# Performance work log

Measured on AMD Instinct MI355X. Metric: run time of the kernel, lower is better.

Reference implementation:

```python
import jax, jax.numpy as jnp
import numpy as np

CLIP = 7.0          # cfg.swiglu_clip
AUX_COEF = 0.02     # cfg.router_aux_loss_coef
TOP_K = 4           # cfg.experts_per_token


def setup_inputs() -> dict:
    key = jax.random.key(0)
    ks = jax.random.split(key, 4)
    H, E, FF = 1024, 16, 1024
    B, T = 2, 1024
    std = 0.02
    return {
        "x": jax.random.normal(ks[0], (B, T, H), jnp.float32),
        "W_in": jax.random.normal(ks[1], (E, H, 2 * FF), jnp.float32) * std,
        "b_in": jnp.zeros((E, 2 * FF), jnp.float32),
        "W_out": jax.random.normal(ks[2], (E, FF, H), jnp.float32) * std,
        "b_out": jnp.zeros((E, H), jnp.float32),
        "router_w": jax.random.normal(ks[3], (E, H), jnp.float32) * std,
        "router_b": jnp.zeros((E,), jnp.float32),
    }


def reference(x, W_in, b_in, W_out, b_out, router_w, router_b):
    B, T, H = x.shape
    E = W_in.shape[0]
    S = B * T
    x_flat = x.reshape(S, H)

    # --- router + top-k gating ---
    logits = x_flat @ router_w.T + router_b                         # [S, E]
    topk_w, topk_i = jax.lax.top_k(logits, TOP_K)                   # [S, K]
    topk_w = jax.nn.softmax(topk_w.astype(jnp.float32), axis=-1).astype(x.dtype)

    # --- aux load-balance loss (faithful to source, incl. argmax-over-indices) ---
    probs = jax.nn.softmax(logits.astype(jnp.float32), axis=-1)     # [S, E]
    importance = probs.mean(axis=0)                                 # [E]
    load = jax.nn.one_hot(jnp.argmax(topk_i, axis=-1), E, dtype=jnp.float32).mean(axis=0)
    aux_loss = AUX_COEF * E * jnp.sum(importance * load)

    # scatter top-k weights to dense [S, E] combine weights
    final_w = jnp.zeros((S, E), x.dtype).at[jnp.arange(S)[:, None], topk_i].add(topk_w)

    # --- dense per-expert SwiGLU FFN (every expert for every token) ---
    h = jnp.einsum('sh,ehd->sed', x_flat, W_in) + b_in              # [S, E, 2*FF]
    up, gate = jnp.split(h, 2, axis=-1)                             # chunk(2, -1)
    up = jnp.clip(up, -CLIP, CLIP)
    gate = jnp.clip(gate, -CLIP, CLIP)
    act = jax.nn.silu(gate) * up                                    # [S, E, FF]
    eo = jnp.einsum('sef,efh->seh', act, W_out) + b_out             # [S, E, H]

    out = jnp.einsum('seh,se->sh', eo, final_w).reshape(B, T, H)
    return out, aux_loss
```

## Files before the change

### kernel.cpp

```cpp
#include <hip/hip_runtime.h>
#include <math.h>

#define S_TOK 2048
#define H_DIM 1024
#define E_NUM 16
#define FF_DIM 1024
#define TOPK 4
#define CLIPV 7.0f
#define AUXC 0.02f
#define BK 32
#define NT (H_DIM / BK)

typedef short bf16x8 __attribute__((ext_vector_type(8)));
typedef float f32x4 __attribute__((ext_vector_type(4)));

__device__ __forceinline__ unsigned short f2bf(float f) {
  unsigned int u = __float_as_uint(f);
  u += 0x7fffu + ((u >> 16) & 1u);
  return (unsigned short)(u >> 16);
}

__device__ __forceinline__ void gload16(const void* g, void* l) {
  __builtin_amdgcn_global_load_lds((const __attribute__((address_space(1))) void*)g,
                                   (__attribute__((address_space(3))) void*)l, 16, 0, 0);
}

__device__ __forceinline__ int imin(int a, int b) { return a < b ? a : b; }

__global__ void logits_kernel(const float* __restrict__ x, const float* __restrict__ rw,
                              const float* __restrict__ rb, float* __restrict__ logits,
                              unsigned short* __restrict__ xb) {
  int tok = blockIdx.x * 4 + (threadIdx.x >> 6);
  int lane = threadIdx.x & 63;
  const float4* xr = (const float4*)(x + (size_t)tok * H_DIM);
  ushort4* xbw = (ushort4*)(xb + (size_t)tok * H_DIM);
  float p[E_NUM];
#pragma unroll
  for (int e = 0; e < E_NUM; ++e) p[e] = 0.f;
#pragma unroll
  for (int it = 0; it < 4; ++it) {
    float4 xv = xr[it * 64 + lane];
    ushort4 o;
    o.x = f2bf(xv.x); o.y = f2bf(xv.y); o.z = f2bf(xv.z); o.w = f2bf(xv.w);
    xbw[it * 64 + lane] = o;
#pragma unroll
    for (int e = 0; e < E_NUM; ++e) {
      float4 wv = ((const float4*)(rw + (size_t)e * H_DIM))[it * 64 + lane];
      p[e] += xv.x * wv.x + xv.y * wv.y + xv.z * wv.z + xv.w * wv.w;
    }
  }
#pragma unroll
  for (int e = 0; e < E_NUM; ++e) {
#pragma unroll
    for (int off = 32; off > 0; off >>= 1) p[e] += __shfl_xor(p[e], off);
  }
  if (lane == 0) {
    float4* lp = (float4*)&logits[tok * E_NUM];
#pragma unroll
    for (int q = 0; q < 4; ++q)
      lp[q] = make_float4(p[q * 4 + 0] + rb[q * 4 + 0], p[q * 4 + 1] + rb[q * 4 + 1],
                          p[q * 4 + 2] + rb[q * 4 + 2], p[q * 4 + 3] + rb[q * 4 + 3]);
  }
}

__global__ __launch_bounds__(256) void topk_kernel(const float* __restrict__ logits,
                                                   int* __restrict__ topk_i, float* __restrict__ topk_w,
                                                   int* __restrict__ counts, float* __restrict__ imp,
                                                   int* __restrict__ pos_cnt) {
  __shared__ float s_imp[E_NUM];
  __shared__ int s_cnt[E_NUM];
  __shared__ int s_pos[TOPK];
  int tid = threadIdx.x;
  if (tid < E_NUM) { s_imp[tid] = 0.f; s_cnt[tid] = 0; }
  if (tid < TOPK) s_pos[tid] = 0;
  __syncthreads();

  int t = blockIdx.x * 256 + tid;
  float lg[E_NUM];
  {
    const float4* lp = (const float4*)&logits[t * E_NUM];
#pragma unroll
    for (int q = 0; q < 4; ++q) {
      float4 v = lp[q];
      lg[q * 4 + 0] = v.x; lg[q * 4 + 1] = v.y; lg[q * 4 + 2] = v.z; lg[q * 4 + 3] = v.w;
    }
  }
  int idx[TOPK]; float val[TOPK];
  float tmp[E_NUM];
#pragma unroll
  for (int e = 0; e < E_NUM; ++e) tmp[e] = lg[e];
#pragma unroll
  for (int k = 0; k < TOPK; ++k) {
    float best = -INFINITY; int bi = 0;
#pragma unroll
    for (int e = 0; e < E_NUM; ++e) if (tmp[e] > best) { best = tmp[e]; bi = e; }
    val[k] = best; idx[k] = bi; tmp[bi] = -INFINITY;
  }
  float ssum = 0.f, wv[TOPK];
#pragma unroll
  for (int k = 0; k < TOPK; ++k) { wv[k] = expf(val[k] - val[0]); ssum += wv[k]; }
#pragma unroll
  for (int k = 0; k < TOPK; ++k) wv[k] /= ssum;
#pragma unroll
  for (int k = 0; k < TOPK; ++k) {
    topk_i[t * TOPK + k] = idx[k];
    topk_w[t * TOPK + k] = wv[k];
  }
  float se = 0.f, pr[E_NUM];
#pragma unroll
  for (int e = 0; e < E_NUM; ++e) { pr[e] = expf(lg[e] - val[0]); se += pr[e]; }
  float inv = 1.f / se;
  int mi = idx[0], pos = 0;
#pragma unroll
  for (int k = 1; k < TOPK; ++k) if (idx[k] > mi) { mi = idx[k]; pos = k; }

  int lane = tid & 63;
#pragma unroll
  for (int e = 0; e < E_NUM; ++e) {
    float v = pr[e] * inv;
    int c = (idx[0] == e) + (idx[1] == e) + (idx[2] == e) + (idx[3] == e);
#pragma unroll
    for (int off = 32; off > 0; off >>= 1) {
      v += __shfl_xor(v, off);
      c += __shfl_xor(c, off);
    }
    if (lane == 0) {
      atomicAdd(&s_imp[e], v);
      atomicAdd(&s_cnt[e], c);
    }
  }
#pragma unroll
  for (int k = 0; k < TOPK; ++k) {
    int pc = (pos == k) ? 1 : 0;
#pragma unroll
    for (int off = 32; off > 0; off >>= 1) pc += __shfl_xor(pc, off);
    if (lane == 0) atomicAdd(&s_pos[k], pc);
  }
  __syncthreads();
  if (tid < E_NUM) {
    atomicAdd(&imp[tid], s_imp[tid]);
    atomicAdd(&counts[tid], s_cnt[tid]);
  }
  if (tid < TOPK) atomicAdd(&pos_cnt[tid], s_pos[tid]);
}

__global__ __launch_bounds__(256) void assign_kernel(
    const int* __restrict__ topk_i, const int* __restrict__ counts, int* __restrict__ cursor,
    int* __restrict__ tok_list, int* __restrict__ slot_of, int* __restrict__ offsets) {
  __shared__ int s_cnt[E_NUM];
  __shared__ int s_base[E_NUM];
  __shared__ int s_off[E_NUM + 1];
  int tid = threadIdx.x;
  if (tid == 0) {
    int o = 0;
    for (int e2 = 0; e2 < E_NUM; ++e2) { s_off[e2] = o; o += counts[e2]; }
    s_off[E_NUM] = o;
    if (blockIdx.x == 0) {
      for (int e2 = 0; e2 <= E_NUM; ++e2) offsets[e2] = s_off[e2];
    }
  }
  if (tid < E_NUM) s_cnt[tid] = 0;
  __syncthreads();
  int t = blockIdx.x * 256 + tid;
  int e[TOPK], lslot[TOPK];
#pragma unroll
  for (int k = 0; k < TOPK; ++k) {
    e[k] = topk_i[t * TOPK + k];
    lslot[k] = atomicAdd(&s_cnt[e[k]], 1);
  }
  __syncthreads();
  if (tid < E_NUM) s_base[tid] = atomicAdd(&cursor[tid], s_cnt[tid]);
  __syncthreads();
#pragma unroll
  for (int k = 0; k < TOPK; ++k) {
    int slot = s_off[e[k]] + s_base[e[k]] + lslot[k];
    tok_list[slot] = t;
    slot_of[t * TOPK + k] = slot;
  }
}

__global__ __launch_bounds__(256, 4) void transpose_fused_kernel(
    const float* __restrict__ W_in, unsigned short* __restrict__ winT,
    const float* __restrict__ W_out, unsigned short* __restrict__ woutT) {
  __shared__ unsigned int tile2[128][66];
  const int bid = blockIdx.x;
  const float* in;
  unsigned short* out;
  int C, r0, c0;
  if (bid < 2048) {
    int e = bid >> 7, rem = bid & 127;
    in  = W_in + (size_t)e * H_DIM * 2 * FF_DIM;
    out = winT + (size_t)e * H_DIM * 2 * FF_DIM;
    C = 2 * FF_DIM;
    r0 = (rem & 7) * 128;
    c0 = (rem >> 3) * 128;
  } else {
    int b = bid - 2048;
    int e = b >> 6, rem = b & 63;
    in  = W_out + (size_t)e * FF_DIM * H_DIM;
    out = woutT + (size_t)e * FF_DIM * H_DIM;
    C = H_DIM;
    r0 = (rem & 7) * 128;
    c0 = (rem >> 3) * 128;
  }
  const int t = threadIdx.x;
  const int tx = t & 31;
  const int ty = t >> 5;
#pragma unroll
  for (int j = 0; j < 8; ++j) {
    int rp = ty + j * 8;
    int r = rp * 2;
    float4 v0 = *(const float4*)&in[(size_t)(r0 + r) * C + c0 + tx * 4];
    float4 v1 = *(const float4*)&in[(size_t)(r0 + r + 1) * C + c0 + tx * 4];
    tile2[tx * 4 + 0][rp] = (unsigned)f2bf(v0.x) | ((unsigned)f2bf(v1.x) << 16);
    tile2[tx * 4 + 1][rp] = (unsigned)f2bf(v0.y) | ((unsigned)f2bf(v1.y) << 16);
    tile2[tx * 4 + 2][rp] = (unsigned)f2bf(v0.z) | ((unsigned)f2bf(v1.z) << 16);
    tile2[tx * 4 + 3][rp] = (unsigned)f2bf(v0.w) | ((unsigned)f2bf(v1.w) << 16);
  }
  __syncthreads();
  const int ux = t & 15;
  const int uy = t >> 4;
#pragma unroll
  for (int j = 0; j < 8; ++j) {
    int c = uy + j * 16;
    uint2 d0 = *(const uint2*)&tile2[c][ux * 4];
    uint2 d1 = *(const uint2*)&tile2[c][ux * 4 + 2];
    uint4 q = make_uint4(d0.x, d0.y, d1.x, d1.y);
    *(uint4*)&out[(size_t)(c0 + c) * 1024 + r0 + ux * 8] = q;
  }
}

__global__ __launch_bounds__(256, 6) void gemm1_kernel(
    const unsigned short* __restrict__ xb, const unsigned short* __restrict__ winT,
    const float* __restrict__ b_in, const int* __restrict__ offsets,
    const int* __restrict__ tok_list, unsigned short* __restrict__ act) {
  __shared__ unsigned short ldsA[2][128 * BK];
  __shared__ unsigned short ldsB[2][64 * BK];
  const int lin = blockIdx.x;
  const int nid = (lin & 7) * 1024 + (lin >> 3);
  const int e  = nid >> 9;
  const int nt = (nid >> 4) & 31;
  const int mt = nid & 15;
  const int base = offsets[e];
  const int cnt = offsets[e + 1] - base;
  if (mt * 128 >= cnt) return;
  const int n0f = nt * 32;
  const int tid = threadIdx.x, w = tid >> 6, lane = tid & 63;

  const int csrc = (lane & 3) ^ ((lane >> 3) & 3);
  const int arow = w * 16 + (lane >> 2);
  const int t0 = tok_list[base + imin(mt * 128 + arow, cnt - 1)];
  const int t1 = tok_list[base + imin(mt * 128 + arow + 64, cnt - 1)];
  const unsigned short* gA0 = xb + (size_t)t0 * H_DIM + csrc * 8;
  const unsigned short* gA1 = xb + (size_t)t1 * H_DIM + csrc * 8;
  const int rB = arow;
  const int fB = n0f + ((rB >> 5) << 4) + (rB & 15);
  const int wrow = ((rB >> 4) & 1) ? (FF_DIM + fB) : fB;
  const unsigned short* we = winT + (size_t)e * 2 * FF_DIM * H_DIM;
  const unsigned short* gB0 = we + (size_t)wrow * H_DIM + csrc * 8;

  f32x4 acc[4][2];
#pragma unroll
  for (int m = 0; m < 4; ++m)
#pragma unroll
    for (int n = 0; n < 2; ++n) acc[m][n] = (f32x4){0.f, 0.f, 0.f, 0.f};

#define STAGE1(buf, k0)                                        \
  do {                                                         \
    gload16(gA0 + (k0), &ldsA[buf][(w * 16) * BK]);            \
    gload16(gA1 + (k0), &ldsA[buf][(w * 16 + 64) * BK]);       \
    gload16(gB0 + (k0), &ldsB[buf][(w * 16) * BK]);            \
  } while (0)

  STAGE1(0, 0);
  __syncthreads();
  int buf = 0;
  const int kos = (((lane >> 4) ^ ((lane >> 1) & 3)) * 8);
  const int wm = (w >> 1) * 64, wn = (w & 1) * 32;
  for (int kt = 0; kt < NT; ++kt) {
    if (kt + 1 < NT) STAGE1(buf ^ 1, (kt + 1) * BK);
    bf16x8 a[4], b[2];
#pragma unroll
    for (int mf = 0; mf < 4; ++mf)
      a[mf] = *(const bf16x8*)&ldsA[buf][(wm + mf * 16 + (lane & 15)) * BK + kos];
#pragma unroll
    for (int nf = 0; nf < 2; ++nf)
      b[nf] = *(const bf16x8*)&ldsB[buf][(wn + nf * 16 + (lane & 15)) * BK + kos];
#pragma unroll
    for (int mf = 0; mf < 4; ++mf)
#pragma unroll
      for (int nf = 0; nf < 2; ++nf)
        acc[mf][nf] = __builtin_amdgcn_mfma_f32_16x16x32_bf16(a[mf], b[nf], acc[mf][nf], 0, 0, 0);
    __syncthreads();
    buf ^= 1;
  }

  const float* bin = b_in + (size_t)e * 2 * FF_DIM;
  const int f = n0f + (w & 1) * 16 + (lane & 15);
  const float bu = bin[f], bg = bin[FF_DIM + f];
#pragma unroll
  for (int mf = 0; mf < 4; ++mf) {
    int rbase = wm + mf * 16 + (lane >> 4) * 4;
#pragma unroll
    for (int i = 0; i < 4; ++i) {
      int mrow = mt * 128 + rbase + i;
      if (mrow < cnt) {
        float up = acc[mf][0][i] + bu;
        float gt = acc[mf][1][i] + bg;
        up = fminf(fmaxf(up, -CLIPV), CLIPV);
        gt = fminf(fmaxf(gt, -CLIPV), CLIPV);
        float av = (gt / (1.f + expf(-gt))) * up;
        act[(size_t)(base + mrow) * FF_DIM + f] = f2bf(av);
      }
    }
  }
}

__global__ __launch_bounds__(256, 4) void gemm2_kernel(
    const unsigned short* __restrict__ act, const unsigned short* __restrict__ woutT,
    const float* __restrict__ b_out, const int* __restrict__ offsets,
    float* __restrict__ eo) {
  __shared__ unsigned short ldsA[2][128 * BK];
  __shared__ unsigned short ldsB[2][128 * BK];
  const int lin = blockIdx.x;
  const int nid = (lin & 7) * 256 + (lin >> 3);
  const int e = nid >> 7;
  const int nt = (nid >> 4) & 7;
  const int mt = nid & 15;
  const int base = offsets[e];
  const int cnt = offsets[e + 1] - base;
  if (mt * 128 >= cnt) return;
  const int n0 = nt * 128;
  const int tid = threadIdx.x, w = tid >> 6, lane = tid & 63;

  const int csrc = (lane & 3) ^ ((lane >> 3) & 3);
  const int srow0 = w * 32 + (lane >> 2);
  const int srow1 = srow0 + 16;
  const int m0_ = imin(mt * 128 + srow0, cnt - 1);
  const int m1_ = imin(mt * 128 + srow1, cnt - 1);
  const unsigned short* gA0 = act + (size_t)(base + m0_) * FF_DIM + csrc * 8;
  const unsigned short* gA1 = act + (size_t)(base + m1_) * FF_DIM + csrc * 8;
  const unsigned short* we = woutT + (size_t)e * H_DIM * FF_DIM;
  const unsigned short* gB0 = we + (size_t)(n0 + srow0) * FF_DIM + csrc * 8;
  const unsigned short* gB1 = we + (size_t)(n0 + srow1) * FF_DIM + csrc * 8;

  f32x4 acc[4][4];
#pragma unroll
  for (int m = 0; m < 4; ++m)
#pragma unroll
    for (int n = 0; n < 4; ++n) acc[m][n] = (f32x4){0.f, 0.f, 0.f, 0.f};

#define STAGE2(buf, k0)                                        \
  do {                                                         \
    gload16(gA0 + (k0), &ldsA[buf][(w * 32 + 0) * BK]);        \
    gload16(gA1 + (k0), &ldsA[buf][(w * 32 + 16) * BK]);       \
    gload16(gB0 + (k0), &ldsB[buf][(w * 32 + 0) * BK]);        \
    gload16(gB1 + (k0), &ldsB[buf][(w * 32 + 16) * BK]);       \
  } while (0)

  STAGE2(0, 0);
  __syncthreads();
  int buf = 0;
  const int kos = (((lane >> 4) ^ ((lane >> 1) & 3)) * 8);
  const int wm = (w >> 1) * 64, wn = (w & 1) * 64;
  for (int kt = 0; kt < FF_DIM / BK; ++kt) {
    if (kt + 1 < FF_DIM / BK) STAGE2(buf ^ 1, (kt + 1) * BK);
    bf16x8 a[4], b[4];
#pragma unroll
    for (int mf = 0; mf < 4; ++mf)
      a[mf] = *(const bf16x8*)&ldsA[buf][(wm + mf * 16 + (lane & 15)) * BK + kos];
#pragma unroll
    for (int nf = 0; nf < 4; ++nf)
      b[nf] = *(const bf16x8*)&ldsB[buf][(wn + nf * 16 + (lane & 15)) * BK + kos];
#pragma unroll
    for (int mf = 0; mf < 4; ++mf)
#pragma unroll
      for (int nf = 0; nf < 4; ++nf)
        acc[mf][nf] = __builtin_amdgcn_mfma_f32_16x16x32_bf16(a[mf], b[nf], acc[mf][nf], 0, 0, 0);
    __syncthreads();
    buf ^= 1;
  }

  const float* bo = b_out + (size_t)e * H_DIM;
#pragma unroll
  for (int mf = 0; mf < 4; ++mf) {
#pragma unroll
    for (int i = 0; i < 4; ++i) {
      int mrow = mt * 128 + wm + mf * 16 + (lane >> 4) * 4 + i;
      if (mrow < cnt) {
        float* row = eo + (size_t)(base + mrow) * H_DIM;
#pragma unroll
        for (int nf = 0; nf < 4; ++nf) {
          int h = n0 + wn + nf * 16 + (lane & 15);
          row[h] = acc[mf][nf][i] + bo[h];
        }
      }
    }
  }
}

__global__ __launch_bounds__(256) void combine_kernel(
    const float* __restrict__ eo, const float* __restrict__ topk_w,
    const int* __restrict__ slot_of, float* __restrict__ out,
    const float* __restrict__ imp, const int* __restrict__ pos_cnt) {
  int t = blockIdx.x;
  int tid = threadIdx.x;
  float4 r = make_float4(0.f, 0.f, 0.f, 0.f);
#pragma unroll
  for (int k = 0; k < TOPK; ++k) {
    int s = slot_of[t * TOPK + k];
    float wv = topk_w[t * TOPK + k];
    float4 v = ((const float4*)(eo + (size_t)s * H_DIM))[tid];
    r.x = fmaf(wv, v.x, r.x);
    r.y = fmaf(wv, v.y, r.y);
    r.z = fmaf(wv, v.z, r.z);
    r.w = fmaf(wv, v.w, r.w);
  }
  ((float4*)(out + (size_t)t * H_DIM))[tid] = r;
  if (t == 0 && tid == 0) {
    float s = 0.f;
    for (int p = 0; p < TOPK; ++p)
      s += (imp[p] / (float)S_TOK) * ((float)pos_cnt[p] / (float)S_TOK);
    out[(size_t)S_TOK * H_DIM] = AUXC * (float)E_NUM * s;
  }
}

extern "C" void kernel_launch(void* const* d_in, const int* in_sizes, int n_in,
                              void* d_out, int out_size, void* d_ws, size_t ws_size,
                              hipStream_t stream) {
  const float* x     = (const float*)d_in[0];
  const float* W_in  = (const float*)d_in[1];
  const float* b_in  = (const float*)d_in[2];
  const float* W_out = (const float*)d_in[3];
  const float* b_out = (const float*)d_in[4];
  const float* rw    = (const float*)d_in[5];
  const float* rb    = (const float*)d_in[6];
  float* out = (float*)d_out;

  char* ws = (char*)d_ws;
  size_t off = 0;
  auto alloc = [&](size_t bytes) {
    void* p = ws + off;
    off = (off + bytes + 255) & ~(size_t)255;
    return p;
  };
  unsigned short* xb    = (unsigned short*)alloc((size_t)S_TOK * H_DIM * 2);
  unsigned short* winT  = (unsigned short*)alloc((size_t)E_NUM * 2 * FF_DIM * H_DIM * 2);
  unsigned short* woutT = (unsigned short*)alloc((size_t)E_NUM * H_DIM * FF_DIM * 2);
  unsigned short* act   = (unsigned short*)alloc((size_t)S_TOK * TOPK * FF_DIM * 2);
  float* eo      = (float*)alloc((size_t)S_TOK * TOPK * H_DIM * 4);
  float* logits  = (float*)alloc((size_t)S_TOK * E_NUM * 4);
  int*   topk_i  = (int*)alloc(S_TOK * TOPK * 4);
  float* topk_w  = (float*)alloc(S_TOK * TOPK * 4);
  int*   tok_list= (int*)alloc(S_TOK * TOPK * 4);
  int*   slot_of = (int*)alloc(S_TOK * TOPK * 4);
  int* ctrl = (int*)alloc(64 * 4);
  int* counts = ctrl;
  int* cursor = ctrl + 16;
  int* pos_cnt = ctrl + 32;
  float* imp = (float*)(ctrl + 48);
  int* offsets = (int*)alloc(32 * 4);

  hipMemsetAsync(ctrl, 0, 64 * 4, stream);

  transpose_fused_kernel<<<3072, 256, 0, stream>>>(W_in, winT, W_out, woutT);
  logits_kernel<<<S_TOK / 4, 256, 0, stream>>>(x, rw, rb, logits, xb);
  topk_kernel<<<S_TOK / 256, 256, 0, stream>>>(logits, topk_i, topk_w, counts, imp, pos_cnt);
  assign_kernel<<<S_TOK / 256, 256, 0, stream>>>(topk_i, counts, cursor, tok_list, slot_of, offsets);
  gemm1_kernel<<<8192, 256, 0, stream>>>(xb, winT, b_in, offsets, tok_list, act);
  gemm2_kernel<<<2048, 256, 0, stream>>>(act, woutT, b_out, offsets, eo);
  combine_kernel<<<S_TOK, 256, 0, stream>>>(eo, topk_w, slot_of, out, imp, pos_cnt);
}
```

Measured before the change: 200.5 us.

## Fuse W_in fp32-to-bf16 conversion into gemm1 and drop its transpose pass

gemm1 now loads the fp32 W_in tiles straight into LDS and converts them to bf16 while building the MFMA B fragments. This removes the separate transpose/convert pass over W_in and the round trip through the winT buffer. The W_out transpose becomes its own kernel launched after gemm1. In exchange, gemm1 reads fp32 weights, twice the bytes, and each active M-tile of an expert rereads them. It also does strided scalar LDS reads plus per-element conversion in the inner loop, and its occupancy hint drops from 6 to 4.

```diff
diff --git a/kernel.cpp b/kernel.cpp
--- a/kernel.cpp
+++ b/kernel.cpp
@@ -179,30 +179,16 @@
   }
 }
 
-__global__ __launch_bounds__(256, 4) void transpose_fused_kernel(
-    const float* __restrict__ W_in, unsigned short* __restrict__ winT,
+__global__ __launch_bounds__(256, 4) void transpose_wout_kernel(
     const float* __restrict__ W_out, unsigned short* __restrict__ woutT) {
   __shared__ unsigned int tile2[128][66];
-  const int bid = blockIdx.x;
-  const float* in;
-  unsigned short* out;
-  int C, r0, c0;
-  if (bid < 2048) {
-    int e = bid >> 7, rem = bid & 127;
-    in  = W_in + (size_t)e * H_DIM * 2 * FF_DIM;
-    out = winT + (size_t)e * H_DIM * 2 * FF_DIM;
-    C = 2 * FF_DIM;
-    r0 = (rem & 7) * 128;
-    c0 = (rem >> 3) * 128;
-  } else {
-    int b = bid - 2048;
-    int e = b >> 6, rem = b & 63;
-    in  = W_out + (size_t)e * FF_DIM * H_DIM;
-    out = woutT + (size_t)e * FF_DIM * H_DIM;
-    C = H_DIM;
-    r0 = (rem & 7) * 128;
-    c0 = (rem >> 3) * 128;
-  }
+  const int b = blockIdx.x;
+  const int e = b >> 6, rem = b & 63;
+  const float* in = W_out + (size_t)e * FF_DIM * H_DIM;
+  unsigned short* out = woutT + (size_t)e * FF_DIM * H_DIM;
+  const int C = H_DIM;
+  const int r0 = (rem & 7) * 128;
+  const int c0 = (rem >> 3) * 128;
   const int t = threadIdx.x;
   const int tx = t & 31;
   const int ty = t >> 5;
@@ -230,12 +216,12 @@
   }
 }
 
-__global__ __launch_bounds__(256, 6) void gemm1_kernel(
-    const unsigned short* __restrict__ xb, const unsigned short* __restrict__ winT,
+__global__ __launch_bounds__(256, 4) void gemm1_kernel(
+    const unsigned short* __restrict__ xb, const float* __restrict__ W_in,
     const float* __restrict__ b_in, const int* __restrict__ offsets,
     const int* __restrict__ tok_list, unsigned short* __restrict__ act) {
   __shared__ unsigned short ldsA[2][128 * BK];
-  __shared__ unsigned short ldsB[2][64 * BK];
+  __shared__ float ldsBf[2][32 * 64];
   const int lin = blockIdx.x;
   const int nid = (lin & 7) * 1024 + (lin >> 3);
   const int e  = nid >> 9;
@@ -253,11 +239,11 @@
   const int t1 = tok_list[base + imin(mt * 128 + arow + 64, cnt - 1)];
   const unsigned short* gA0 = xb + (size_t)t0 * H_DIM + csrc * 8;
   const unsigned short* gA1 = xb + (size_t)t1 * H_DIM + csrc * 8;
-  const int rB = arow;
-  const int fB = n0f + ((rB >> 5) << 4) + (rB & 15);
-  const int wrow = ((rB >> 4) & 1) ? (FF_DIM + fB) : fB;
-  const unsigned short* we = winT + (size_t)e * 2 * FF_DIM * H_DIM;
-  const unsigned short* gB0 = we + (size_t)wrow * H_DIM + csrc * 8;
+
+  const int q = lane & 15;
+  const int btype = (q >> 2) & 1;
+  const int colb = (btype ? FF_DIM : 0) + n0f + ((q >> 3) << 4) + 4 * (q & 3);
+  const float* pB = W_in + (size_t)e * H_DIM * 2 * FF_DIM + colb + (size_t)(lane >> 4) * (2 * FF_DIM);
 
   f32x4 acc[4][2];
 #pragma unroll
@@ -265,17 +251,21 @@
 #pragma unroll
     for (int n = 0; n < 2; ++n) acc[m][n] = (f32x4){0.f, 0.f, 0.f, 0.f};
 
-#define STAGE1(buf, k0)                                        \
-  do {                                                         \
-    gload16(gA0 + (k0), &ldsA[buf][(w * 16) * BK]);            \
-    gload16(gA1 + (k0), &ldsA[buf][(w * 16 + 64) * BK]);       \
-    gload16(gB0 + (k0), &ldsB[buf][(w * 16) * BK]);            \
+#define STAGE1(buf, k0)                                                          \
+  do {                                                                           \
+    gload16(gA0 + (k0), &ldsA[buf][(w * 16) * BK]);                              \
+    gload16(gA1 + (k0), &ldsA[buf][(w * 16 + 64) * BK]);                         \
+    gload16(pB + (size_t)((k0) + w * 4) * (2 * FF_DIM),                          \
+            (char*)&ldsBf[buf][0] + w * 1024);                                   \
+    gload16(pB + (size_t)((k0) + 16 + w * 4) * (2 * FF_DIM),                     \
+            (char*)&ldsBf[buf][0] + 4096 + w * 1024);                            \
   } while (0)
 
   STAGE1(0, 0);
   __syncthreads();
   int buf = 0;
   const int kos = (((lane >> 4) ^ ((lane >> 1) & 3)) * 8);
+  const int kol = (lane >> 4) * 8;
   const int wm = (w >> 1) * 64, wn = (w & 1) * 32;
   for (int kt = 0; kt < NT; ++kt) {
     if (kt + 1 < NT) STAGE1(buf ^ 1, (kt + 1) * BK);
@@ -284,8 +274,13 @@
     for (int mf = 0; mf < 4; ++mf)
       a[mf] = *(const bf16x8*)&ldsA[buf][(wm + mf * 16 + (lane & 15)) * BK + kos];
 #pragma unroll
-    for (int nf = 0; nf < 2; ++nf)
-      b[nf] = *(const bf16x8*)&ldsB[buf][(wn + nf * 16 + (lane & 15)) * BK + kos];
+    for (int nf = 0; nf < 2; ++nf) {
+      const float* bp = &ldsBf[buf][(size_t)kol * 64 + wn + nf * 16 + (lane & 15)];
+      bf16x8 bb;
+#pragma unroll
+      for (int j = 0; j < 8; ++j) bb[j] = (short)f2bf(bp[j * 64]);
+      b[nf] = bb;
+    }
 #pragma unroll
     for (int mf = 0; mf < 4; ++mf)
 #pragma unroll
@@ -445,7 +440,6 @@
     return p;
   };
   unsigned short* xb    = (unsigned short*)alloc((size_t)S_TOK * H_DIM * 2);
-  unsigned short* winT  = (unsigned short*)alloc((size_t)E_NUM * 2 * FF_DIM * H_DIM * 2);
   unsigned short* woutT = (unsigned short*)alloc((size_t)E_NUM * H_DIM * FF_DIM * 2);
   unsigned short* act   = (unsigned short*)alloc((size_t)S_TOK * TOPK * FF_DIM * 2);
   float* eo      = (float*)alloc((size_t)S_TOK * TOPK * H_DIM * 4);
@@ -463,11 +457,11 @@
 
   hipMemsetAsync(ctrl, 0, 64 * 4, stream);
 
-  transpose_fused_kernel<<<3072, 256, 0, stream>>>(W_in, winT, W_out, woutT);
   logits_kernel<<<S_TOK / 4, 256, 0, stream>>>(x, rw, rb, logits, xb);
   topk_kernel<<<S_TOK / 256, 256, 0, stream>>>(logits, topk_i, topk_w, counts, imp, pos_cnt);
   assign_kernel<<<S_TOK / 256, 256, 0, stream>>>(topk_i, counts, cursor, tok_list, slot_of, offsets);
-  gemm1_kernel<<<8192, 256, 0, stream>>>(xb, winT, b_in, offsets, tok_list, act);
+  gemm1_kernel<<<8192, 256, 0, stream>>>(xb, W_in, b_in, offsets, tok_list, act);
+  transpose_wout_kernel<<<1024, 256, 0, stream>>>(W_out, woutT);
   gemm2_kernel<<<2048, 256, 0, stream>>>(act, woutT, b_out, offsets, eo);
   combine_kernel<<<S_TOK, 256, 0, stream>>>(eo, topk_w, slot_of, out, imp, pos_cnt);
 }
```

Measured after the change: 262.2 us. 1.31x slower.
